# Kernel tuning notes

Measured on AMD Instinct MI355X. Metric: run time of the kernel, lower is better.

## Reference

```python
import jax, jax.numpy as jnp
import numpy as np

EPS = 1e-7  # K.epsilon()
ROUTINGS = 3

def squash(v, axis=-1):
    s2 = jnp.sum(jnp.square(v), axis=axis, keepdims=True)
    scale = s2 / (1.0 + s2) / jnp.sqrt(s2 + EPS)
    return scale * v

def setup_inputs() -> dict:
    key = jax.random.key(0)
    k1, k2 = jax.random.split(key)
    B, N, I = 128, 512, 256   # batch, input_num_capsule, input_dim_capsule
    M, D = 32, 16             # num_capsule, dim_capsule
    x = jax.random.normal(k1, (B, N, I), dtype=jnp.float32)
    W = jax.random.normal(k2, (M, N, D, I), dtype=jnp.float32) * 0.05
    return {"x": x, "W": W}

def reference(x, W):
    # x: [B,N,I], W: [M,N,D,I]
    # inputs_hat[b,m,n,d] = sum_i x[b,n,i] * W[m,n,d,i]
    inputs_hat = jnp.einsum('bni,mndi->bmnd', x, W)
    B, M, N, _ = inputs_hat.shape
    b = jnp.zeros((B, M, N), dtype=inputs_hat.dtype)
    outputs = None
    for i in range(ROUTINGS):
        c = jax.nn.softmax(b, axis=1)  # softmax over num_capsule dim (dim=1)
        s = jnp.einsum('bmn,bmnd->bmd', c, inputs_hat)
        outputs = squash(s)
        if i < ROUTINGS - 1:
            b = b + jnp.einsum('bmd,bmnd->bmn', outputs, inputs_hat)
    return outputs
```

## Files before the change

kernel.cpp:

```cpp
#include <hip/hip_runtime.h>
#include <stdint.h>

#define B_ 128
#define N_ 512
#define I_ 256
#define M_ 32
#define D_ 16

typedef __attribute__((ext_vector_type(4))) float f32x4;
typedef __attribute__((ext_vector_type(4))) float float4v;
typedef __attribute__((ext_vector_type(8))) short short8;
typedef __attribute__((ext_vector_type(4))) unsigned short ushort4v;

__device__ __forceinline__ float bf2f(unsigned short u) {
    union { unsigned int i; float f; } v; v.i = ((unsigned int)u) << 16; return v.f;
}
__device__ __forceinline__ unsigned short f2bf(float f) {
    union { float f; unsigned int i; } v; v.f = f;
    unsigned int r = v.i + 0x7FFFu + ((v.i >> 16) & 1u);
    return (unsigned short)(r >> 16);
}

#define LDK 72

__global__ __launch_bounds__(256, 4) void hat_gemm(const float* __restrict__ x,
                                                   const float* __restrict__ W,
                                                   unsigned short* __restrict__ hat) {
    __shared__ unsigned short As[128][LDK];
    __shared__ unsigned short Bs[64][LDK];

    const int L   = blockIdx.x;
    const int xcd = L & 7;
    const int i   = L >> 3;
    const int n   = xcd * 64 + (i >> 3);
    const int mc  = i & 7;

    const int tid  = threadIdx.x;
    const int lane = tid & 63;
    const int w    = tid >> 6;
    const int l15  = lane & 15;

    const int sgrp  = tid >> 4;
    const int klane = (tid & 15) * 4;

    const float* xrow = x + ((size_t)sgrp * N_ + n) * I_ + klane;
    const float* wrow = W + (((size_t)(mc * 4) * N_ + n) * D_ + sgrp) * I_ + klane;
    const size_t xstep = (size_t)16 * N_ * I_;
    const size_t wstep = (size_t)N_ * D_ * I_;

    float4v pa[8], pb[4];

    f32x4 acc[2][4];
    #pragma unroll
    for (int a = 0; a < 2; ++a)
        #pragma unroll
        for (int c = 0; c < 4; ++c) { f32x4 z = {0.f, 0.f, 0.f, 0.f}; acc[a][c] = z; }

    #pragma unroll
    for (int r = 0; r < 8; ++r) pa[r] = *(const float4v*)(xrow + (size_t)r * xstep);
    #pragma unroll
    for (int r = 0; r < 4; ++r) pb[r] = *(const float4v*)(wrow + (size_t)r * wstep);

    for (int kt = 0; kt < 4; ++kt) {
        #pragma unroll
        for (int r = 0; r < 8; ++r) {
            ushort4v h;
            h[0] = f2bf(pa[r][0]); h[1] = f2bf(pa[r][1]);
            h[2] = f2bf(pa[r][2]); h[3] = f2bf(pa[r][3]);
            *(ushort4v*)&As[r * 16 + sgrp][klane] = h;
        }
        #pragma unroll
        for (int r = 0; r < 4; ++r) {
            ushort4v h;
            h[0] = f2bf(pb[r][0]); h[1] = f2bf(pb[r][1]);
            h[2] = f2bf(pb[r][2]); h[3] = f2bf(pb[r][3]);
            *(ushort4v*)&Bs[r * 16 + sgrp][klane] = h;
        }
        __syncthreads();

        if (kt < 3) {
            const int k0 = (kt + 1) * 64;
            #pragma unroll
            for (int r = 0; r < 8; ++r)
                pa[r] = *(const float4v*)(xrow + (size_t)r * xstep + k0);
            #pragma unroll
            for (int r = 0; r < 4; ++r)
                pb[r] = *(const float4v*)(wrow + (size_t)r * wstep + k0);
        }

        #pragma unroll
        for (int ks = 0; ks < 2; ++ks) {
            const int kb = ks * 32 + ((lane >> 4) << 3);
            short8 a0 = *(const short8*)&As[w * 32 +      l15][kb];
            short8 a1 = *(const short8*)&As[w * 32 + 16 + l15][kb];
            #pragma unroll
            for (int ct = 0; ct < 4; ++ct) {
                short8 bb = *(const short8*)&Bs[ct * 16 + l15][kb];
                acc[0][ct] = __builtin_amdgcn_mfma_f32_16x16x32_bf16(a0, bb, acc[0][ct], 0, 0, 0);
                acc[1][ct] = __builtin_amdgcn_mfma_f32_16x16x32_bf16(a1, bb, acc[1][ct], 0, 0, 0);
            }
        }
        __syncthreads();
    }

    const int d  = l15;
    const int rq = lane >> 4;
    #pragma unroll
    for (int rt = 0; rt < 2; ++rt) {
        #pragma unroll
        for (int ct = 0; ct < 4; ++ct) {
            const int m = mc * 4 + ct;
            #pragma unroll
            for (int r = 0; r < 4; ++r) {
                const int brow = w * 32 + rt * 16 + rq * 4 + r;
                const size_t idx = (((size_t)brow * M_ + m) * N_ + n) * D_ + d;
                hat[idx] = f2bf(acc[rt][ct][r]);
            }
        }
    }
}

__global__ __launch_bounds__(512) void routing(const unsigned short* __restrict__ hat,
                                               float* __restrict__ out) {
    __shared__ float blog[M_][N_];
    __shared__ float cmax[N_];
    __shared__ float rcsum[N_];

    const int b    = blockIdx.x;
    const int tid  = threadIdx.x;
    const int lane = tid & 63;
    const int w    = tid >> 6;

    #pragma unroll
    for (int m = 0; m < M_; ++m) blog[m][tid] = 0.f;
    __syncthreads();

    float ov[4][16];

    for (int it = 0; it < 3; ++it) {
        {
            float mx = -3.4e38f;
            #pragma unroll
            for (int m = 0; m < M_; ++m) mx = fmaxf(mx, blog[m][tid]);
            float s = 0.f;
            #pragma unroll
            for (int m = 0; m < M_; ++m) s += __expf(blog[m][tid] - mx);
            cmax[tid]  = mx;
            rcsum[tid] = 1.f / s;
        }
        __syncthreads();

        float sacc[4][16];
        #pragma unroll
        for (int q = 0; q < 4; ++q)
            #pragma unroll
            for (int dd = 0; dd < 16; ++dd) sacc[q][dd] = 0.f;

        for (int r = 0; r < 8; ++r) {
            const int nn = r * 64 + lane;
            #pragma unroll
            for (int q = 0; q < 4; ++q) {
                const int m = w * 4 + q;
                const float cm = __expf(blog[m][nn] - cmax[nn]) * rcsum[nn];
                const size_t base = (((size_t)b * M_ + m) * N_ + nn) * D_;
                short8 h0 = *(const short8*)(hat + base);
                short8 h1 = *(const short8*)(hat + base + 8);
                #pragma unroll
                for (int dd = 0; dd < 8; ++dd) {
                    sacc[q][dd]     += cm * bf2f((unsigned short)h0[dd]);
                    sacc[q][8 + dd] += cm * bf2f((unsigned short)h1[dd]);
                }
            }
        }
        #pragma unroll
        for (int off = 32; off >= 1; off >>= 1) {
            #pragma unroll
            for (int q = 0; q < 4; ++q)
                #pragma unroll
                for (int dd = 0; dd < 16; ++dd)
                    sacc[q][dd] += __shfl_xor(sacc[q][dd], off, 64);
        }
        #pragma unroll
        for (int q = 0; q < 4; ++q) {
            float s2 = 0.f;
            #pragma unroll
            for (int dd = 0; dd < 16; ++dd) s2 += sacc[q][dd] * sacc[q][dd];
            const float scale = s2 / (1.f + s2) / sqrtf(s2 + 1e-7f);
            #pragma unroll
            for (int dd = 0; dd < 16; ++dd) ov[q][dd] = scale * sacc[q][dd];
        }

        if (it < 2) {
            for (int r = 0; r < 8; ++r) {
                const int nn = r * 64 + lane;
                #pragma unroll
                for (int q = 0; q < 4; ++q) {
                    const int m = w * 4 + q;
                    const size_t base = (((size_t)b * M_ + m) * N_ + nn) * D_;
                    short8 h0 = *(const short8*)(hat + base);
                    short8 h1 = *(const short8*)(hat + base + 8);
                    float dot = 0.f;
                    #pragma unroll
                    for (int dd = 0; dd < 8; ++dd) {
                        dot += ov[q][dd]     * bf2f((unsigned short)h0[dd]);
                        dot += ov[q][8 + dd] * bf2f((unsigned short)h1[dd]);
                    }
                    blog[m][nn] += dot;
                }
            }
        }
        __syncthreads();
    }

    if (lane == 0) {
        #pragma unroll
        for (int q = 0; q < 4; ++q) {
            const int m = w * 4 + q;
            #pragma unroll
            for (int c4 = 0; c4 < 4; ++c4) {
                float4v v;
                v[0] = ov[q][c4 * 4 + 0];
                v[1] = ov[q][c4 * 4 + 1];
                v[2] = ov[q][c4 * 4 + 2];
                v[3] = ov[q][c4 * 4 + 3];
                *(float4v*)&out[((size_t)b * M_ + m) * D_ + c4 * 4] = v;
            }
        }
    }
}

extern "C" void kernel_launch(void* const* d_in, const int* in_sizes, int n_in,
                              void* d_out, int out_size, void* d_ws, size_t ws_size,
                              hipStream_t stream) {
    const float* x = (const float*)d_in[0];
    const float* W = (const float*)d_in[1];
    unsigned short* hat = (unsigned short*)d_ws;
    float* out = (float*)d_out;

    hat_gemm<<<dim3(4096), dim3(256), 0, stream>>>(x, W, hat);
    routing<<<dim3(B_), dim3(512), 0, stream>>>(hat, out);
}
```

Baseline: 183.7 us.

## Double-buffer global loads in hat_gemm with inline asm and manual waitcnt barriers

The K loop of the hat GEMM is fully unrolled with two register sets (pa/pb and qa/qb). The next tile's global loads are issued as inline-asm dwordx4 loads, with explicit vmcnt/lgkmcnt waits and sched barriers, so loads stay in flight across the LDS conversion and MFMA phases. Launch bounds drop from 4 to 3 waves per SIMD to make room for the extra registers. The cost is lower occupancy, plus a risk that vmcnt(0) waits serialize more than intended. Because the asm loads are opaque, the compiler can no longer schedule around them.

```diff
diff --git a/kernel.cpp b/kernel.cpp
--- a/kernel.cpp
+++ b/kernel.cpp
@@ -21,9 +21,30 @@
     return (unsigned short)(r >> 16);
 }
 
+#define GLOAD16(dst, ptr) \
+    asm volatile("global_load_dwordx4 %0, %1, off" : "=&v"(dst) : "v"(ptr))
+
+#define VMWAIT0() do { \
+    asm volatile("s_waitcnt vmcnt(0)" ::: "memory"); \
+    __builtin_amdgcn_sched_barrier(0); \
+} while (0)
+
+#define LGKM0_BARRIER() do { \
+    asm volatile("s_waitcnt lgkmcnt(0)" ::: "memory"); \
+    __builtin_amdgcn_sched_barrier(0); \
+    __builtin_amdgcn_s_barrier(); \
+    __builtin_amdgcn_sched_barrier(0); \
+} while (0)
+
+#define BARRIER() do { \
+    __builtin_amdgcn_sched_barrier(0); \
+    __builtin_amdgcn_s_barrier(); \
+    __builtin_amdgcn_sched_barrier(0); \
+} while (0)
+
 #define LDK 72
 
-__global__ __launch_bounds__(256, 4) void hat_gemm(const float* __restrict__ x,
+__global__ __launch_bounds__(256, 3) void hat_gemm(const float* __restrict__ x,
                                                    const float* __restrict__ W,
                                                    unsigned short* __restrict__ hat) {
     __shared__ unsigned short As[128][LDK];
@@ -48,7 +69,7 @@
     const size_t xstep = (size_t)16 * N_ * I_;
     const size_t wstep = (size_t)N_ * D_ * I_;
 
-    float4v pa[8], pb[4];
+    float4v pa[8], pb[4], qa[8], qb[4];
 
     f32x4 acc[2][4];
     #pragma unroll
@@ -56,52 +77,72 @@
         #pragma unroll
         for (int c = 0; c < 4; ++c) { f32x4 z = {0.f, 0.f, 0.f, 0.f}; acc[a][c] = z; }
 
-    #pragma unroll
-    for (int r = 0; r < 8; ++r) pa[r] = *(const float4v*)(xrow + (size_t)r * xstep);
-    #pragma unroll
-    for (int r = 0; r < 4; ++r) pb[r] = *(const float4v*)(wrow + (size_t)r * wstep);
-
-    for (int kt = 0; kt < 4; ++kt) {
-        #pragma unroll
-        for (int r = 0; r < 8; ++r) {
-            ushort4v h;
-            h[0] = f2bf(pa[r][0]); h[1] = f2bf(pa[r][1]);
-            h[2] = f2bf(pa[r][2]); h[3] = f2bf(pa[r][3]);
-            *(ushort4v*)&As[r * 16 + sgrp][klane] = h;
-        }
-        #pragma unroll
-        for (int r = 0; r < 4; ++r) {
-            ushort4v h;
-            h[0] = f2bf(pb[r][0]); h[1] = f2bf(pb[r][1]);
-            h[2] = f2bf(pb[r][2]); h[3] = f2bf(pb[r][3]);
-            *(ushort4v*)&Bs[r * 16 + sgrp][klane] = h;
-        }
-        __syncthreads();
-
-        if (kt < 3) {
-            const int k0 = (kt + 1) * 64;
-            #pragma unroll
-            for (int r = 0; r < 8; ++r)
-                pa[r] = *(const float4v*)(xrow + (size_t)r * xstep + k0);
-            #pragma unroll
-            for (int r = 0; r < 4; ++r)
-                pb[r] = *(const float4v*)(wrow + (size_t)r * wstep + k0);
-        }
-
-        #pragma unroll
-        for (int ks = 0; ks < 2; ++ks) {
-            const int kb = ks * 32 + ((lane >> 4) << 3);
-            short8 a0 = *(const short8*)&As[w * 32 +      l15][kb];
-            short8 a1 = *(const short8*)&As[w * 32 + 16 + l15][kb];
-            #pragma unroll
-            for (int ct = 0; ct < 4; ++ct) {
-                short8 bb = *(const short8*)&Bs[ct * 16 + l15][kb];
-                acc[0][ct] = __builtin_amdgcn_mfma_f32_16x16x32_bf16(a0, bb, acc[0][ct], 0, 0, 0);
-                acc[1][ct] = __builtin_amdgcn_mfma_f32_16x16x32_bf16(a1, bb, acc[1][ct], 0, 0, 0);
-            }
-        }
-        __syncthreads();
-    }
+    #define ISSUE(va, vb, k0) do { \
+        _Pragma("unroll") \
+        for (int r = 0; r < 8; ++r) GLOAD16(va[r], xrow + (size_t)r * xstep + (k0)); \
+        _Pragma("unroll") \
+        for (int r = 0; r < 4; ++r) GLOAD16(vb[r], wrow + (size_t)r * wstep + (k0)); \
+    } while (0)
+
+    #define CONVERT(va, vb) do { \
+        _Pragma("unroll") \
+        for (int r = 0; r < 8; ++r) { \
+            ushort4v h; \
+            h[0] = f2bf(va[r][0]); h[1] = f2bf(va[r][1]); \
+            h[2] = f2bf(va[r][2]); h[3] = f2bf(va[r][3]); \
+            *(ushort4v*)&As[r * 16 + sgrp][klane] = h; \
+        } \
+        _Pragma("unroll") \
+        for (int r = 0; r < 4; ++r) { \
+            ushort4v h; \
+            h[0] = f2bf(vb[r][0]); h[1] = f2bf(vb[r][1]); \
+            h[2] = f2bf(vb[r][2]); h[3] = f2bf(vb[r][3]); \
+            *(ushort4v*)&Bs[r * 16 + sgrp][klane] = h; \
+        } \
+    } while (0)
+
+    #define MFMA_TILE() do { \
+        _Pragma("unroll") \
+        for (int ks = 0; ks < 2; ++ks) { \
+            const int kb = ks * 32 + ((lane >> 4) << 3); \
+            short8 a0 = *(const short8*)&As[w * 32 +      l15][kb]; \
+            short8 a1 = *(const short8*)&As[w * 32 + 16 + l15][kb]; \
+            _Pragma("unroll") \
+            for (int ct = 0; ct < 4; ++ct) { \
+                short8 bb = *(const short8*)&Bs[ct * 16 + l15][kb]; \
+                acc[0][ct] = __builtin_amdgcn_mfma_f32_16x16x32_bf16(a0, bb, acc[0][ct], 0, 0, 0); \
+                acc[1][ct] = __builtin_amdgcn_mfma_f32_16x16x32_bf16(a1, bb, acc[1][ct], 0, 0, 0); \
+            } \
+        } \
+    } while (0)
+
+    ISSUE(pa, pb, 0);
+
+    VMWAIT0();
+    CONVERT(pa, pb);
+    ISSUE(qa, qb, 64);
+    LGKM0_BARRIER();
+    MFMA_TILE();
+    BARRIER();
+
+    VMWAIT0();
+    CONVERT(qa, qb);
+    ISSUE(pa, pb, 128);
+    LGKM0_BARRIER();
+    MFMA_TILE();
+    BARRIER();
+
+    VMWAIT0();
+    CONVERT(pa, pb);
+    ISSUE(qa, qb, 192);
+    LGKM0_BARRIER();
+    MFMA_TILE();
+    BARRIER();
+
+    VMWAIT0();
+    CONVERT(qa, qb);
+    LGKM0_BARRIER();
+    MFMA_TILE();
 
     const int d  = l15;
     const int rq = lane >> 4;
@@ -118,6 +159,9 @@
             }
         }
     }
+    #undef ISSUE
+    #undef CONVERT
+    #undef MFMA_TILE
 }
 
 __global__ __launch_bounds__(512) void routing(const unsigned short* __restrict__ hat,
```

Measured after the change: 188.8 us. 2.8% more time.
